# Optimization experiments

Measured on AMD Instinct MI355X. Metric: run time of the kernel, lower is better.

## Reference

```python
import jax, jax.numpy as jnp
import numpy as np

B, D, K = 4, 64, 32
T, H, W = 8, 32, 32


def setup_inputs() -> dict:
    key = jax.random.key(0)
    k1, k2, k3, k4, k5 = jax.random.split(key, 5)
    std1 = 1.0 / float(np.sqrt(K * D))
    X = jax.random.normal(k1, (B, D, T, H, W), dtype=jnp.float32)
    codewords = jax.random.uniform(k2, (K, D), dtype=jnp.float32, minval=-std1, maxval=std1)
    scale = jax.random.uniform(k3, (K, D), dtype=jnp.float32, minval=-1.0, maxval=0.0)
    fc_w = jax.random.normal(k4, (D, D), dtype=jnp.float32) * (1.0 / np.sqrt(D))
    fc_b = jax.random.normal(k5, (D,), dtype=jnp.float32) * 0.01
    return {"X": X, "codewords": codewords, "scale": scale, "fc_w": fc_w, "fc_b": fc_b}


def reference(X, codewords, scale, fc_w, fc_b):
    b, d, t, h, w = X.shape
    n = t * h * w
    # (B, N, D) voxel features
    I = X.reshape(b, d, n).transpose(0, 2, 1)
    # residuals to each codeword: (B, N, K, D)
    resid = I[:, :, None, :] - codewords[None, None, :, :]
    # scaled squared-distance softmax over K (per feature channel d)
    A = jax.nn.softmax(scale[None, None, :, :] * jnp.square(resid), axis=2)
    AR = A * resid  # (B, N, K, D)
    # aggregate over voxels -> (B, K, D), then mean over codewords -> (B, D)
    E_glob = AR.sum(axis=1).mean(axis=1)
    gamma = jax.nn.sigmoid(E_glob @ fc_w.T + fc_b)  # (B, D)
    # aggregate over codewords -> (B, N, D) -> (B, D, T, H, W)
    E = AR.sum(axis=2).transpose(0, 2, 1).reshape(b, d, t, h, w)
    return jax.nn.relu(E + E * gamma[:, :, None, None, None])
```

## Files before the change

kernel.cpp:

```cpp
#include <hip/hip_runtime.h>
#include <hip/hip_bf16.h>

#define BB 4
#define DD 64
#define KK 32
#define NN 8192
#define LOG2E 1.4426950408889634f

__global__ __launch_bounds__(256) void enc_kernel(
    const float* __restrict__ X,
    const float* __restrict__ cw,
    const float* __restrict__ sc,
    float* __restrict__ E,
    float* __restrict__ partial)
{
    const int bd   = blockIdx.x >> 3;
    const int d    = bd & (DD - 1);
    const int idx  = bd * NN + (blockIdx.x & 7) * 1024 + (threadIdx.x << 2);

    const float4 x = *(const float4*)(X + idx);

    float num0 = 0.f, num1 = 0.f, num2 = 0.f, num3 = 0.f;
    float den0 = 0.f, den1 = 0.f, den2 = 0.f, den3 = 0.f;

#pragma unroll
    for (int k = 0; k < KK; ++k) {
        const float c = cw[k * DD + d];
        const float s = sc[k * DD + d] * LOG2E;
        const float r0 = x.x - c;
        const float r1 = x.y - c;
        const float r2 = x.z - c;
        const float r3 = x.w - c;
        const float e0 = exp2f(s * r0 * r0);
        const float e1 = exp2f(s * r1 * r1);
        const float e2 = exp2f(s * r2 * r2);
        const float e3 = exp2f(s * r3 * r3);
        den0 += e0; num0 = fmaf(e0, r0, num0);
        den1 += e1; num1 = fmaf(e1, r1, num1);
        den2 += e2; num2 = fmaf(e2, r2, num2);
        den3 += e3; num3 = fmaf(e3, r3, num3);
    }

    float4 out;
    out.x = num0 / den0;
    out.y = num1 / den1;
    out.z = num2 / den2;
    out.w = num3 / den3;
    *(float4*)(E + idx) = out;

    float t = out.x + out.y + out.z + out.w;
#pragma unroll
    for (int off = 32; off > 0; off >>= 1)
        t += __shfl_down(t, off);

    __shared__ float smem[4];
    if ((threadIdx.x & 63) == 0) smem[threadIdx.x >> 6] = t;
    __syncthreads();
    if (threadIdx.x == 0)
        partial[blockIdx.x] = smem[0] + smem[1] + smem[2] + smem[3];
}

__global__ __launch_bounds__(256) void gate_kernel(
    float* __restrict__ E,
    const float* __restrict__ partial,
    const float* __restrict__ fcw,
    const float* __restrict__ fcb)
{
    const int bd  = blockIdx.x >> 3;
    const int b   = bd >> 6;
    const int d   = bd & (DD - 1);
    const int idx = bd * NN + (blockIdx.x & 7) * 1024 + (threadIdx.x << 2);

    __shared__ float eg[DD];
    if (threadIdx.x < DD) {
        const float4* p = (const float4*)(partial + b * 512 + threadIdx.x * 8);
        const float4 a = p[0], c4 = p[1];
        eg[threadIdx.x] = (a.x + a.y + a.z + a.w) + (c4.x + c4.y + c4.z + c4.w);
    }
    float4 e = *(float4*)(E + idx);
    __syncthreads();

    float acc = 0.f;
#pragma unroll
    for (int j = 0; j < DD; ++j)
        acc = fmaf(eg[j], fcw[d * DD + j], acc);
    const float z = acc * (1.0f / (float)KK) + fcb[d];
    const float g = 1.0f + 1.0f / (1.0f + exp2f(-z * LOG2E));

    e.x = fmaxf(e.x * g, 0.f);
    e.y = fmaxf(e.y * g, 0.f);
    e.z = fmaxf(e.z * g, 0.f);
    e.w = fmaxf(e.w * g, 0.f);
    *(float4*)(E + idx) = e;
}

extern "C" void kernel_launch(void* const* d_in, const int* in_sizes, int n_in,
                              void* d_out, int out_size, void* d_ws, size_t ws_size,
                              hipStream_t stream) {
    const float* X   = (const float*)d_in[0];
    const float* cw  = (const float*)d_in[1];
    const float* sc  = (const float*)d_in[2];
    const float* fcw = (const float*)d_in[3];
    const float* fcb = (const float*)d_in[4];
    float* out = (float*)d_out;

    float* partial = (float*)d_ws;

    const int grid = BB * DD * (NN / 1024);
    enc_kernel<<<grid, 256, 0, stream>>>(X, cw, sc, out, partial);
    gate_kernel<<<grid, 256, 0, stream>>>(out, partial, fcw, fcb);
}
```

Baseline: 90.48 us.

## Fuse encoding and gating into one cooperative kernel with grid sync

Merges the encode and gate kernels into one cooperative launch that keeps each thread's E values in registers across a grid-wide sync. This avoids writing E to global memory and reading it back, and saves a second kernel launch. Each thread now handles 8 voxels with half as many blocks, and the exponent is rewritten as a*x^2 + b*x + c so only a weighted codeword sum is accumulated. The cost is a grid barrier and the requirement that all 1024 blocks be co-resident; the rewritten quadratic may also lose some precision through cancellation.

```diff
diff --git a/kernel.cpp b/kernel.cpp
--- a/kernel.cpp
+++ b/kernel.cpp
@@ -1,5 +1,5 @@
 #include <hip/hip_runtime.h>
-#include <hip/hip_bf16.h>
+#include <hip/hip_cooperative_groups.h>
 
 #define BB 4
 #define DD 64
@@ -7,77 +7,67 @@
 #define NN 8192
 #define LOG2E 1.4426950408889634f
 
-__global__ __launch_bounds__(256) void enc_kernel(
+namespace cg = cooperative_groups;
+
+__global__ __launch_bounds__(256, 4) void fused_kernel(
     const float* __restrict__ X,
     const float* __restrict__ cw,
     const float* __restrict__ sc,
-    float* __restrict__ E,
+    const float* __restrict__ fcw,
+    const float* __restrict__ fcb,
+    float* __restrict__ out,
     float* __restrict__ partial)
 {
-    const int bd   = blockIdx.x >> 3;
-    const int d    = bd & (DD - 1);
-    const int idx  = bd * NN + (blockIdx.x & 7) * 1024 + (threadIdx.x << 2);
+    const int bd    = blockIdx.x >> 2;
+    const int b     = bd >> 6;
+    const int d     = bd & (DD - 1);
+    const int base  = bd * NN + (blockIdx.x & 3) * 2048 + (threadIdx.x << 3);
 
-    const float4 x = *(const float4*)(X + idx);
+    const float4 xa = *(const float4*)(X + base);
+    const float4 xb = *(const float4*)(X + base + 4);
+    float xs[8] = {xa.x, xa.y, xa.z, xa.w, xb.x, xb.y, xb.z, xb.w};
 
-    float num0 = 0.f, num1 = 0.f, num2 = 0.f, num3 = 0.f;
-    float den0 = 0.f, den1 = 0.f, den2 = 0.f, den3 = 0.f;
+    float den[8] = {0,0,0,0,0,0,0,0};
+    float cn[8]  = {0,0,0,0,0,0,0,0};
 
 #pragma unroll
     for (int k = 0; k < KK; ++k) {
-        const float c = cw[k * DD + d];
-        const float s = sc[k * DD + d] * LOG2E;
-        const float r0 = x.x - c;
-        const float r1 = x.y - c;
-        const float r2 = x.z - c;
-        const float r3 = x.w - c;
-        const float e0 = exp2f(s * r0 * r0);
-        const float e1 = exp2f(s * r1 * r1);
-        const float e2 = exp2f(s * r2 * r2);
-        const float e3 = exp2f(s * r3 * r3);
-        den0 += e0; num0 = fmaf(e0, r0, num0);
-        den1 += e1; num1 = fmaf(e1, r1, num1);
-        den2 += e2; num2 = fmaf(e2, r2, num2);
-        den3 += e3; num3 = fmaf(e3, r3, num3);
+        const float c  = cw[k * DD + d];
+        const float a  = sc[k * DD + d] * LOG2E;
+        const float b2 = -2.0f * a * c;
+        const float c2 = a * c * c;
+#pragma unroll
+        for (int i = 0; i < 8; ++i) {
+            const float e = exp2f(fmaf(fmaf(a, xs[i], b2), xs[i], c2));
+            den[i] += e;
+            cn[i]   = fmaf(e, c, cn[i]);
+        }
     }
 
-    float4 out;
-    out.x = num0 / den0;
-    out.y = num1 / den1;
-    out.z = num2 / den2;
-    out.w = num3 / den3;
-    *(float4*)(E + idx) = out;
+    float E[8];
+    float t = 0.f;
+#pragma unroll
+    for (int i = 0; i < 8; ++i) {
+        E[i] = xs[i] - cn[i] / den[i];
+        t += E[i];
+    }
 
-    float t = out.x + out.y + out.z + out.w;
 #pragma unroll
     for (int off = 32; off > 0; off >>= 1)
         t += __shfl_down(t, off);
-
     __shared__ float smem[4];
+    __shared__ float eg[DD];
     if ((threadIdx.x & 63) == 0) smem[threadIdx.x >> 6] = t;
     __syncthreads();
     if (threadIdx.x == 0)
         partial[blockIdx.x] = smem[0] + smem[1] + smem[2] + smem[3];
-}
 
-__global__ __launch_bounds__(256) void gate_kernel(
-    float* __restrict__ E,
-    const float* __restrict__ partial,
-    const float* __restrict__ fcw,
-    const float* __restrict__ fcb)
-{
-    const int bd  = blockIdx.x >> 3;
-    const int b   = bd >> 6;
-    const int d   = bd & (DD - 1);
-    const int idx = bd * NN + (blockIdx.x & 7) * 1024 + (threadIdx.x << 2);
+    cg::this_grid().sync();
 
-    __shared__ float eg[DD];
     if (threadIdx.x < DD) {
-        const float4* p = (const float4*)(partial + b * 512 + threadIdx.x * 8);
-        const float4 a = p[0], c4 = p[1];
-        eg[threadIdx.x] = (a.x + a.y + a.z + a.w) + (c4.x + c4.y + c4.z + c4.w);
+        const float4 p = *(const float4*)(partial + (b * DD + threadIdx.x) * 4);
+        eg[threadIdx.x] = p.x + p.y + p.z + p.w;
     }
-    float4 e = *(float4*)(E + idx);
     __syncthreads();
 
     float acc = 0.f;
@@ -87,11 +77,13 @@
     const float z = acc * (1.0f / (float)KK) + fcb[d];
     const float g = 1.0f + 1.0f / (1.0f + exp2f(-z * LOG2E));
 
-    e.x = fmaxf(e.x * g, 0.f);
-    e.y = fmaxf(e.y * g, 0.f);
-    e.z = fmaxf(e.z * g, 0.f);
-    e.w = fmaxf(e.w * g, 0.f);
-    *(float4*)(E + idx) = e;
+    float4 oa, ob;
+    oa.x = fmaxf(E[0] * g, 0.f); oa.y = fmaxf(E[1] * g, 0.f);
+    oa.z = fmaxf(E[2] * g, 0.f); oa.w = fmaxf(E[3] * g, 0.f);
+    ob.x = fmaxf(E[4] * g, 0.f); ob.y = fmaxf(E[5] * g, 0.f);
+    ob.z = fmaxf(E[6] * g, 0.f); ob.w = fmaxf(E[7] * g, 0.f);
+    *(float4*)(out + base)     = oa;
+    *(float4*)(out + base + 4) = ob;
 }
 
 extern "C" void kernel_launch(void* const* d_in, const int* in_sizes, int n_in,
@@ -102,11 +94,12 @@
     const float* sc  = (const float*)d_in[2];
     const float* fcw = (const float*)d_in[3];
     const float* fcb = (const float*)d_in[4];
-    float* out = (float*)d_out;
+    float* out       = (float*)d_out;
+    float* partial   = (float*)d_ws;
 
-    float* partial = (float*)d_ws;
-
-    const int grid = BB * DD * (NN / 1024);
-    enc_kernel<<<grid, 256, 0, stream>>>(X, cw, sc, out, partial);
-    gate_kernel<<<grid, 256, 0, stream>>>(out, partial, fcw, fcb);
+    void* args[] = {(void*)&X, (void*)&cw, (void*)&sc, (void*)&fcw,
+                    (void*)&fcb, (void*)&out, (void*)&partial};
+    hipLaunchCooperativeKernel((const void*)fused_kernel,
+                               dim3(BB * DD * 4), dim3(256),
+                               args, 0, stream);
 }
```

After: 157.5 us. 1.74x slower.
